# Optimization experiments

Measured on AMD Instinct MI355X. Metric: run time of the kernel, lower is better.

## Reference

```python
import jax, jax.numpy as jnp
import numpy as np

TOP_K = 2
EPS = 1e-9

def setup_inputs() -> dict:
    key = jax.random.key(0)
    ks = jax.random.split(key, 8)
    B, L, C, F = 64, 512, 3, 300          # batteries, cycles, channels, curve length
    d_model, d_llm, d_ff, E = 512, 4096, 2048, 8
    s = lambda k, sh: jax.random.normal(k, sh, jnp.float32) * 0.02
    return dict(
        cycle_curve_data=jax.random.normal(ks[0], (B, L, C, F), jnp.float32),
        cycle_numbers=jax.random.uniform(ks[1], (B, 1), jnp.float32),
        DKP_embeddings=jax.random.normal(ks[2], (B, d_llm), jnp.float32),
        gate_W1=s(ks[3], (d_llm + 1, d_ff)), gate_b1=jnp.zeros((d_ff,), jnp.float32),
        gate_W2=s(ks[4], (d_ff, E)), gate_b2=jnp.zeros((E,), jnp.float32),
        expert_W=s(ks[5], (E, C * F, d_model)), expert_b=jnp.zeros((E, d_model), jnp.float32),
        gen_W=s(ks[6], (C * F, d_model)), gen_b=jnp.zeros((d_model,), jnp.float32),
    )

def reference(cycle_curve_data, cycle_numbers, DKP_embeddings,
              gate_W1, gate_b1, gate_W2, gate_b2,
              expert_W, expert_b, gen_W, gen_b):
    B, L, C, F = cycle_curve_data.shape
    # router (PatternRouter_two): 2-layer MLP over [DKP embedding ; cycle number]
    g_in = jnp.concatenate([DKP_embeddings, cycle_numbers], axis=-1)   # [B, d_llm+1]
    h = jax.nn.gelu(g_in @ gate_W1 + gate_b1)
    logits = h @ gate_W2 + gate_b2                                     # [B, E]
    # top-k mask on raw logits (as in source), softmax, mask, renormalize
    _, idx = jax.lax.top_k(logits, TOP_K)
    mask = jnp.zeros(logits.shape, bool).at[jnp.arange(B)[:, None], idx].set(True)
    p = jax.nn.softmax(logits, axis=1)
    g = jnp.where(mask, p, 0.0)
    gates = g / (jnp.sum(g, axis=1, keepdims=True) + EPS)              # [B, E]
    # experts: flatten(start_dim=2) then Linear(3*F -> d_model); combine is linear
    # so fold gates into a per-battery weight: sum_e gates[b,e] * W_e
    x = cycle_curve_data.reshape(B, L, C * F)                          # [B, L, 3F]
    Wb = jnp.einsum('be,eid->bid', gates, expert_W)                    # [B, 3F, d]
    bb = gates @ expert_b                                              # [B, d]
    moe_out = jnp.einsum('bli,bid->bld', x, Wb) + bb[:, None, :]       # [B, L, d]
    general = x @ gen_W + gen_b                                        # [B, L, d]
    # source casts the combined MoE output to bf16 before adding
    return general + moe_out.astype(jnp.bfloat16)
```

## Files before the change

kernel.cpp:

```cpp
#include <hip/hip_runtime.h>
#include <hip/hip_bf16.h>
#include <stdint.h>

typedef __attribute__((ext_vector_type(8))) short short8;
typedef __attribute__((ext_vector_type(4))) short short4v;
typedef __attribute__((ext_vector_type(4))) float f32x4;

__device__ inline unsigned short f2bf(float f) {
    union { float f; uint32_t u; } v; v.f = f;
    uint32_t u = v.u;
    uint32_t r = (u + 0x7FFFu + ((u >> 16) & 1u)) >> 16;
    return (unsigned short)r;
}

__device__ inline short4v pk4(float4 a) {
    short4v r;
    r[0] = (short)f2bf(a.x); r[1] = (short)f2bf(a.y);
    r[2] = (short)f2bf(a.z); r[3] = (short)f2bf(a.w);
    return r;
}

__global__ __launch_bounds__(256) void router1(const float* __restrict__ DKP,
                                               const float* __restrict__ W1,
                                               float* __restrict__ part) {
    __shared__ float gin[16 * 64];
    const int t  = threadIdx.x;
    const int lin = blockIdx.x + 16 * blockIdx.y;
    const int bg  = (lin >> 3) & 3;
    const int grp = (lin & 7) | ((lin >> 5) << 3);
    const int jc  = grp & 3;
    const int ks  = grp >> 2;
    const int k0 = ks * 64;
    {
        const int b = t >> 4, q = t & 15;
        *(float4*)(gin + b * 64 + q * 4) =
            *(const float4*)(DKP + (size_t)(bg * 16 + b) * 4096 + k0 + q * 4);
    }
    __syncthreads();
    const int ja = jc * 512 + t, jb = ja + 256;
    float accA[16], accB[16];
    #pragma unroll
    for (int b = 0; b < 16; ++b) { accA[b] = 0.f; accB[b] = 0.f; }
    #pragma unroll 1
    for (int oct = 0; oct < 8; ++oct) {
        const int kk = oct * 8;
        float wa[8], wb[8];
        #pragma unroll
        for (int i = 0; i < 8; ++i) {
            const float* wr = W1 + (size_t)(k0 + kk + i) * 2048;
            wa[i] = wr[ja]; wb[i] = wr[jb];
        }
        #pragma unroll
        for (int b = 0; b < 16; ++b) {
            float4 g0 = *(const float4*)(gin + b * 64 + kk);
            float4 g1 = *(const float4*)(gin + b * 64 + kk + 4);
            accA[b] += g0.x*wa[0] + g0.y*wa[1] + g0.z*wa[2] + g0.w*wa[3]
                     + g1.x*wa[4] + g1.y*wa[5] + g1.z*wa[6] + g1.w*wa[7];
            accB[b] += g0.x*wb[0] + g0.y*wb[1] + g0.z*wb[2] + g0.w*wb[3]
                     + g1.x*wb[4] + g1.y*wb[5] + g1.z*wb[6] + g1.w*wb[7];
        }
    }
    #pragma unroll 1
    for (int b = 0; b < 16; ++b) {
        const size_t row = (size_t)(ks * 64 + bg * 16 + b) * 2048;
        part[row + ja] = accA[b];
        part[row + jb] = accB[b];
    }
}

__global__ __launch_bounds__(256) void router2(const float* __restrict__ part,
                                               const float* __restrict__ cyc,
                                               const float* __restrict__ W1,
                                               const float* __restrict__ b1,
                                               float* __restrict__ h) {
    const int idx = blockIdx.x * 256 + threadIdx.x;
    const int j = idx & 2047, b = idx >> 11;
    float s = 0.f;
    #pragma unroll 8
    for (int t = 0; t < 64; ++t)
        s += part[((size_t)t * 64 + b) * 2048 + j];
    s += cyc[b] * W1[(size_t)4096 * 2048 + j] + b1[j];
    const float u  = s + 0.044715f * s * s * s;
    const float th = tanhf(0.7978845608028654f * u);
    h[idx] = 0.5f * s * (1.0f + th);
}

__global__ __launch_bounds__(256) void router3(const float* __restrict__ h,
                                               const float* __restrict__ W2,
                                               const float* __restrict__ b2,
                                               float4* __restrict__ gates) {
    __shared__ float red[256 * 8];
    __shared__ float lg[8];
    const int b = blockIdx.x, t = threadIdx.x;
    float acc[8];
    #pragma unroll
    for (int e = 0; e < 8; ++e) acc[e] = 0.f;
    for (int k = t; k < 2048; k += 256) {
        const float hv = h[(size_t)b * 2048 + k];
        const float* w = W2 + (size_t)k * 8;
        #pragma unroll
        for (int e = 0; e < 8; ++e) acc[e] += hv * w[e];
    }
    #pragma unroll
    for (int e = 0; e < 8; ++e) red[t * 8 + e] = acc[e];
    __syncthreads();
    if (t < 8) {
        float s = 0.f;
        for (int r = 0; r < 256; ++r) s += red[r * 8 + t];
        lg[t] = s + b2[t];
    }
    __syncthreads();
    if (t == 0) {
        float l[8];
        #pragma unroll
        for (int e = 0; e < 8; ++e) l[e] = lg[e];
        int e0 = 0;
        #pragma unroll
        for (int e = 1; e < 8; ++e) if (l[e] > l[e0]) e0 = e;
        int e1 = (e0 == 0) ? 1 : 0;
        #pragma unroll
        for (int e = 0; e < 8; ++e) if (e != e0 && l[e] > l[e1]) e1 = e;
        const float m = l[e0];
        float p[8], Z = 0.f;
        #pragma unroll
        for (int e = 0; e < 8; ++e) { p[e] = expf(l[e] - m); Z += p[e]; }
        const float pe0 = p[e0] / Z, pe1 = p[e1] / Z;
        const float s2 = pe0 + pe1 + 1e-9f;
        gates[b] = make_float4(__int_as_float(e0), __int_as_float(e1), pe0 / s2, pe1 / s2);
    }
}

__global__ __launch_bounds__(256) void combine_w(const float* __restrict__ genW,
                                                 const float* __restrict__ expW,
                                                 const float4* __restrict__ gates,
                                                 unsigned short* __restrict__ wc) {
    __shared__ unsigned short T[64 * 72];
    const int b  = blockIdx.z;
    const int i0 = blockIdx.y * 64;
    const int d0 = blockIdx.x * 64;
    const float4 gt = gates[b];
    const int e0 = __float_as_int(gt.x), e1 = __float_as_int(gt.y);
    const float g0 = gt.z, g1 = gt.w;
    const float* W0 = expW + (size_t)e0 * 900 * 512;
    const float* W1e = expW + (size_t)e1 * 900 * 512;
    const int t = threadIdx.x;
    {
        const int il = t >> 2, c = t & 3;
        const int i = i0 + il;
        const bool valid = (i < 900);
        const size_t rowoff = (size_t)i * 512 + d0 + c * 16;
        #pragma unroll
        for (int s = 0; s < 4; ++s) {
            float4 g  = valid ? *(const float4*)(genW + rowoff + 4 * s) : make_float4(0,0,0,0);
            float4 w0 = valid ? *(const float4*)(W0   + rowoff + 4 * s) : make_float4(0,0,0,0);
            float4 w1 = valid ? *(const float4*)(W1e  + rowoff + 4 * s) : make_float4(0,0,0,0);
            const int dl = c * 16 + 4 * s;
            T[(dl + 0) * 72 + il] = f2bf(g.x + g0 * w0.x + g1 * w1.x);
            T[(dl + 1) * 72 + il] = f2bf(g.y + g0 * w0.y + g1 * w1.y);
            T[(dl + 2) * 72 + il] = f2bf(g.z + g0 * w0.z + g1 * w1.z);
            T[(dl + 3) * 72 + il] = f2bf(g.w + g0 * w0.w + g1 * w1.w);
        }
    }
    __syncthreads();
    {
        const int dl = t >> 2, seg = t & 3;
        const int ic = seg * 16;
        if (i0 + ic < 928) {
            short8 v0 = *(const short8*)&T[dl * 72 + ic];
            short8 v1 = *(const short8*)&T[dl * 72 + ic + 8];
            unsigned short* dst = wc + (size_t)b * 512 * 928 + (size_t)(d0 + dl) * 928 + i0 + ic;
            *(short8*)dst = v0;
            *((short8*)dst + 1) = v1;
        }
    }
}

__global__ __launch_bounds__(512, 4) void moe_gemm(const float* __restrict__ x,
                                                   const unsigned short* __restrict__ wc,
                                                   const float4* __restrict__ gates,
                                                   const float* __restrict__ eb,
                                                   const float* __restrict__ genb,
                                                   float* __restrict__ out) {
    __shared__ unsigned short As[2][64 * 40];
    __shared__ unsigned short Bs[2][512 * 32];
    const int b  = blockIdx.x;
    const int m0 = blockIdx.y * 64;
    const int t = threadIdx.x, lane = t & 63, wid = t >> 6;
    const float4 gt = gates[b];
    const int e0 = __float_as_int(gt.x), e1 = __float_as_int(gt.y);
    const float g0 = gt.z, g1 = gt.w;
    const float* xb = x + (size_t)b * 512 * 900;
    const unsigned short* wcb = wc + (size_t)b * 512 * 928;
    f32x4 acc[4][4];
    #pragma unroll
    for (int mi = 0; mi < 4; ++mi)
        #pragma unroll
        for (int ni = 0; ni < 4; ++ni)
            acc[mi][ni] = (f32x4){0.f, 0.f, 0.f, 0.f};

    const int arow  = t >> 3;
    const int akoff = (t & 7) * 4;
    const float* xrow = xb + (size_t)(m0 + arow) * 900 + akoff;
    const int bseg = (lane & 3) ^ ((lane >> 3) & 3);
    const int burow = lane >> 2;

    const int wn = wid * 64;
    const int lm = lane & 15, lq = lane >> 4;

    auto loadA = [&](int kt) -> float4 {
        if (kt < 28) return *(const float4*)(xrow + kt * 32);
        float4 z = make_float4(0.f, 0.f, 0.f, 0.f);
        if (akoff == 0) z = *(const float4*)(xrow + 896);
        return z;
    };
    auto stageB = [&](int buf, int kt) {
        const int k0 = kt * 32;
        #pragma unroll
        for (int r = 0; r < 4; ++r) {
            const int chunk = wid * 4 + r;
            const int n = chunk * 16 + burow;
            const unsigned short* gsrc = wcb + (size_t)n * 928 + k0 + bseg * 8;
            unsigned short* ldst = &Bs[buf][chunk * 512];
            __builtin_amdgcn_global_load_lds(
                (const __attribute__((address_space(1))) unsigned int*)gsrc,
                (__attribute__((address_space(3))) unsigned int*)ldst, 16, 0, 0);
        }
    };
    auto packA = [&](int buf, float4 f) {
        *(short4v*)&As[buf][arow * 40 + akoff] = pk4(f);
    };
    auto compute = [&](int buf) {
        short8 af[4], bfr[4];
        #pragma unroll
        for (int mi = 0; mi < 4; ++mi)
            af[mi] = *(const short8*)&As[buf][(mi * 16 + lm) * 40 + lq * 8];
        #pragma unroll
        for (int ni = 0; ni < 4; ++ni) {
            const int n = wn + ni * 16 + lm;
            const int slot = lq ^ ((lm >> 1) & 3);
            bfr[ni] = *(const short8*)&Bs[buf][n * 32 + slot * 8];
        }
        #pragma unroll
        for (int mi = 0; mi < 4; ++mi)
            #pragma unroll
            for (int ni = 0; ni < 4; ++ni)
                acc[mi][ni] = __builtin_amdgcn_mfma_f32_16x16x32_bf16(
                    af[mi], bfr[ni], acc[mi][ni], 0, 0, 0);
    };

    {
        float4 a0 = loadA(0);
        stageB(0, 0);
        packA(0, a0);
        __syncthreads();
    }
    #pragma unroll 1
    for (int kt2 = 0; kt2 < 14; ++kt2) {
        {
            float4 an = loadA(2 * kt2 + 1);
            stageB(1, 2 * kt2 + 1);
            compute(0);
            packA(1, an);
            __syncthreads();
        }
        {
            float4 an = loadA(2 * kt2 + 2);
            stageB(0, 2 * kt2 + 2);
            compute(1);
            packA(0, an);
            __syncthreads();
        }
    }
    compute(0);

    #pragma unroll
    for (int ni = 0; ni < 4; ++ni) {
        const int col = wn + ni * 16 + lm;
        const float bias = genb[col] + g0 * eb[e0 * 512 + col] + g1 * eb[e1 * 512 + col];
        #pragma unroll
        for (int mi = 0; mi < 4; ++mi) {
            const int row = m0 + mi * 16 + lq * 4;
            #pragma unroll
            for (int r = 0; r < 4; ++r)
                out[((size_t)b * 512 + row + r) * 512 + col] = acc[mi][ni][r] + bias;
        }
    }
}

extern "C" void kernel_launch(void* const* d_in, const int* in_sizes, int n_in,
                              void* d_out, int out_size, void* d_ws, size_t ws_size,
                              hipStream_t stream) {
    const float* x    = (const float*)d_in[0];
    const float* cyc  = (const float*)d_in[1];
    const float* dkp  = (const float*)d_in[2];
    const float* gW1  = (const float*)d_in[3];
    const float* gb1  = (const float*)d_in[4];
    const float* gW2  = (const float*)d_in[5];
    const float* gb2  = (const float*)d_in[6];
    const float* eW   = (const float*)d_in[7];
    const float* eb   = (const float*)d_in[8];
    const float* genW = (const float*)d_in[9];
    const float* genb = (const float*)d_in[10];
    float* out = (float*)d_out;

    char* ws = (char*)d_ws;
    unsigned short* wcomb = (unsigned short*)ws;
    float* part  = (float*)ws;
    float* h     = (float*)(ws + 60817408);
    float4* gts  = (float4*)(ws + 60817408 + 524288);

    router1<<<dim3(16, 64), 256, 0, stream>>>(dkp, gW1, part);
    router2<<<512, 256, 0, stream>>>(part, cyc, gW1, gb1, h);
    router3<<<64, 256, 0, stream>>>(h, gW2, gb2, gts);
    combine_w<<<dim3(8, 15, 64), 256, 0, stream>>>(genW, eW, gts, wcomb);
    moe_gemm<<<dim3(64, 8), 512, 0, stream>>>(x, wcomb, gts, eb, genb, out);
}
```

Measured before the change: 376.3 us.

## Fuse router stages, reuse expert weights across batches, and pipeline MoE GEMM waits

The router's first stage now uses deeper K slices (fewer partial sums), and the reduction/GELU stage is fused into the logits/top-k kernel, removing one launch and the h buffer. The weight-combine kernel loads all nine weight matrices for a tile once into shared memory and loops over all 64 batteries, instead of re-reading global weights per battery. The MoE GEMM main loop replaces __syncthreads with explicit s_waitcnt vmcnt(1) barriers plus sched_barriers, prefetching A two tiles ahead so global loads overlap compute. The risks are fewer router blocks for parallelism, higher shared memory use in combine_w, and hand-written waitcnt logic that could hide a race.

```diff
diff --git a/kernel.cpp b/kernel.cpp
--- a/kernel.cpp
+++ b/kernel.cpp
@@ -23,81 +23,70 @@
 __global__ __launch_bounds__(256) void router1(const float* __restrict__ DKP,
                                                const float* __restrict__ W1,
                                                float* __restrict__ part) {
-    __shared__ float gin[16 * 64];
-    const int t  = threadIdx.x;
+    __shared__ float gin[16 * 256];
+    const int t   = threadIdx.x;
     const int lin = blockIdx.x + 16 * blockIdx.y;
+    const int jc  = lin & 7;
     const int bg  = (lin >> 3) & 3;
-    const int grp = (lin & 7) | ((lin >> 5) << 3);
-    const int jc  = grp & 3;
-    const int ks  = grp >> 2;
-    const int k0 = ks * 64;
+    const int ks  = lin >> 5;
+    const int k0  = ks * 256;
     {
         const int b = t >> 4, q = t & 15;
-        *(float4*)(gin + b * 64 + q * 4) =
-            *(const float4*)(DKP + (size_t)(bg * 16 + b) * 4096 + k0 + q * 4);
+        #pragma unroll
+        for (int s = 0; s < 4; ++s)
+            *(float4*)(gin + b * 256 + q * 16 + s * 4) =
+                *(const float4*)(DKP + (size_t)(bg * 16 + b) * 4096 + k0 + q * 16 + s * 4);
     }
     __syncthreads();
-    const int ja = jc * 512 + t, jb = ja + 256;
-    float accA[16], accB[16];
-    #pragma unroll
-    for (int b = 0; b < 16; ++b) { accA[b] = 0.f; accB[b] = 0.f; }
-    #pragma unroll 1
-    for (int oct = 0; oct < 8; ++oct) {
+    const int ja = jc * 256 + t;
+    float accA[16];
+    #pragma unroll
+    for (int b = 0; b < 16; ++b) accA[b] = 0.f;
+    #pragma unroll 1
+    for (int oct = 0; oct < 32; ++oct) {
         const int kk = oct * 8;
-        float wa[8], wb[8];
-        #pragma unroll
-        for (int i = 0; i < 8; ++i) {
-            const float* wr = W1 + (size_t)(k0 + kk + i) * 2048;
-            wa[i] = wr[ja]; wb[i] = wr[jb];
-        }
+        float wa[8];
+        #pragma unroll
+        for (int i = 0; i < 8; ++i)
+            wa[i] = W1[(size_t)(k0 + kk + i) * 2048 + ja];
         #pragma unroll
         for (int b = 0; b < 16; ++b) {
-            float4 g0 = *(const float4*)(gin + b * 64 + kk);
-            float4 g1 = *(const float4*)(gin + b * 64 + kk + 4);
+            float4 g0 = *(const float4*)(gin + b * 256 + kk);
+            float4 g1 = *(const float4*)(gin + b * 256 + kk + 4);
             accA[b] += g0.x*wa[0] + g0.y*wa[1] + g0.z*wa[2] + g0.w*wa[3]
                      + g1.x*wa[4] + g1.y*wa[5] + g1.z*wa[6] + g1.w*wa[7];
-            accB[b] += g0.x*wb[0] + g0.y*wb[1] + g0.z*wb[2] + g0.w*wb[3]
-                     + g1.x*wb[4] + g1.y*wb[5] + g1.z*wb[6] + g1.w*wb[7];
-        }
-    }
-    #pragma unroll 1
-    for (int b = 0; b < 16; ++b) {
-        const size_t row = (size_t)(ks * 64 + bg * 16 + b) * 2048;
-        part[row + ja] = accA[b];
-        part[row + jb] = accB[b];
-    }
-}
-
-__global__ __launch_bounds__(256) void router2(const float* __restrict__ part,
-                                               const float* __restrict__ cyc,
-                                               const float* __restrict__ W1,
-                                               const float* __restrict__ b1,
-                                               float* __restrict__ h) {
-    const int idx = blockIdx.x * 256 + threadIdx.x;
-    const int j = idx & 2047, b = idx >> 11;
-    float s = 0.f;
-    #pragma unroll 8
-    for (int t = 0; t < 64; ++t)
-        s += part[((size_t)t * 64 + b) * 2048 + j];
-    s += cyc[b] * W1[(size_t)4096 * 2048 + j] + b1[j];
-    const float u  = s + 0.044715f * s * s * s;
-    const float th = tanhf(0.7978845608028654f * u);
-    h[idx] = 0.5f * s * (1.0f + th);
-}
-
-__global__ __launch_bounds__(256) void router3(const float* __restrict__ h,
-                                               const float* __restrict__ W2,
-                                               const float* __restrict__ b2,
-                                               float4* __restrict__ gates) {
+        }
+    }
+    #pragma unroll 1
+    for (int b = 0; b < 16; ++b)
+        part[((size_t)(ks * 64 + bg * 16 + b)) * 2048 + ja] = accA[b];
+}
+
+__global__ __launch_bounds__(256) void router23(const float* __restrict__ part,
+                                                const float* __restrict__ cyc,
+                                                const float* __restrict__ W1,
+                                                const float* __restrict__ b1,
+                                                const float* __restrict__ W2,
+                                                const float* __restrict__ b2,
+                                                float4* __restrict__ gates) {
     __shared__ float red[256 * 8];
     __shared__ float lg[8];
     const int b = blockIdx.x, t = threadIdx.x;
     float acc[8];
     #pragma unroll
     for (int e = 0; e < 8; ++e) acc[e] = 0.f;
-    for (int k = t; k < 2048; k += 256) {
-        const float hv = h[(size_t)b * 2048 + k];
-        const float* w = W2 + (size_t)k * 8;
+    #pragma unroll 1
+    for (int jj = 0; jj < 8; ++jj) {
+        const int j = jj * 256 + t;
+        float s = 0.f;
+        #pragma unroll
+        for (int tt = 0; tt < 16; ++tt)
+            s += part[((size_t)tt * 64 + b) * 2048 + j];
+        s += cyc[b] * W1[(size_t)4096 * 2048 + j] + b1[j];
+        const float u  = s + 0.044715f * s * s * s;
+        const float th = tanhf(0.7978845608028654f * u);
+        const float hv = 0.5f * s * (1.0f + th);
+        const float* w = W2 + (size_t)j * 8;
         #pragma unroll
         for (int e = 0; e < 8; ++e) acc[e] += hv * w[e];
     }
@@ -134,44 +123,46 @@
                                                  const float* __restrict__ expW,
                                                  const float4* __restrict__ gates,
                                                  unsigned short* __restrict__ wc) {
-    __shared__ unsigned short T[64 * 72];
-    const int b  = blockIdx.z;
-    const int i0 = blockIdx.y * 64;
-    const int d0 = blockIdx.x * 64;
-    const float4 gt = gates[b];
-    const int e0 = __float_as_int(gt.x), e1 = __float_as_int(gt.y);
-    const float g0 = gt.z, g1 = gt.w;
-    const float* W0 = expW + (size_t)e0 * 900 * 512;
-    const float* W1e = expW + (size_t)e1 * 900 * 512;
-    const int t = threadIdx.x;
+    __shared__ float T[9][32 * 36];
+    __shared__ float4 gsh[64];
+    const int t  = threadIdx.x;
+    const int d0 = blockIdx.x * 32;
+    const int i0 = blockIdx.y * 32;
+    if (t < 64) gsh[t] = gates[t];
     {
-        const int il = t >> 2, c = t & 3;
+        const int il = t >> 3, d4 = (t & 7) * 4;
         const int i = i0 + il;
         const bool valid = (i < 900);
-        const size_t rowoff = (size_t)i * 512 + d0 + c * 16;
-        #pragma unroll
-        for (int s = 0; s < 4; ++s) {
-            float4 g  = valid ? *(const float4*)(genW + rowoff + 4 * s) : make_float4(0,0,0,0);
-            float4 w0 = valid ? *(const float4*)(W0   + rowoff + 4 * s) : make_float4(0,0,0,0);
-            float4 w1 = valid ? *(const float4*)(W1e  + rowoff + 4 * s) : make_float4(0,0,0,0);
-            const int dl = c * 16 + 4 * s;
-            T[(dl + 0) * 72 + il] = f2bf(g.x + g0 * w0.x + g1 * w1.x);
-            T[(dl + 1) * 72 + il] = f2bf(g.y + g0 * w0.y + g1 * w1.y);
-            T[(dl + 2) * 72 + il] = f2bf(g.z + g0 * w0.z + g1 * w1.z);
-            T[(dl + 3) * 72 + il] = f2bf(g.w + g0 * w0.w + g1 * w1.w);
+        const size_t off = (size_t)i * 512 + d0 + d4;
+        #pragma unroll
+        for (int s = 0; s < 9; ++s) {
+            const float* src = (s == 0) ? genW : (expW + (size_t)(s - 1) * 900 * 512);
+            float4 v = valid ? *(const float4*)(src + off) : make_float4(0, 0, 0, 0);
+            float* Td = &T[s][0];
+            Td[(d4 + 0) * 36 + il] = v.x;
+            Td[(d4 + 1) * 36 + il] = v.y;
+            Td[(d4 + 2) * 36 + il] = v.z;
+            Td[(d4 + 3) * 36 + il] = v.w;
         }
     }
     __syncthreads();
-    {
-        const int dl = t >> 2, seg = t & 3;
-        const int ic = seg * 16;
-        if (i0 + ic < 928) {
-            short8 v0 = *(const short8*)&T[dl * 72 + ic];
-            short8 v1 = *(const short8*)&T[dl * 72 + ic + 8];
-            unsigned short* dst = wc + (size_t)b * 512 * 928 + (size_t)(d0 + dl) * 928 + i0 + ic;
-            *(short8*)dst = v0;
-            *((short8*)dst + 1) = v1;
-        }
+    const int dl = t >> 3, sg = t & 7;
+    const int fo = dl * 36 + sg * 4;
+    unsigned short* wrow = wc + (size_t)(d0 + dl) * 928 + i0 + sg * 4;
+    #pragma unroll 1
+    for (int b = 0; b < 64; ++b) {
+        const float4 gt = gsh[b];
+        const int e0 = __float_as_int(gt.x), e1 = __float_as_int(gt.y);
+        const float g0 = gt.z, g1 = gt.w;
+        float4 G = *(const float4*)&T[0][fo];
+        float4 X = *(const float4*)&T[1 + e0][fo];
+        float4 Y = *(const float4*)&T[1 + e1][fo];
+        short4v r;
+        r[0] = (short)f2bf(G.x + g0 * X.x + g1 * Y.x);
+        r[1] = (short)f2bf(G.y + g0 * X.y + g1 * Y.y);
+        r[2] = (short)f2bf(G.z + g0 * X.z + g1 * Y.z);
+        r[3] = (short)f2bf(G.w + g0 * X.w + g1 * Y.w);
+        *(short4v*)(wrow + (size_t)b * 512 * 928) = r;
     }
 }
 
@@ -248,30 +239,64 @@
                     af[mi], bfr[ni], acc[mi][ni], 0, 0, 0);
     };
 
+#define BAR_V1() do { \
+    asm volatile("s_waitcnt vmcnt(1) lgkmcnt(0)\n\ts_barrier" ::: "memory"); \
+    __builtin_amdgcn_sched_barrier(0); } while (0)
+#define BAR_V0() do { \
+    asm volatile("s_waitcnt vmcnt(0) lgkmcnt(0)\n\ts_barrier" ::: "memory"); \
+    __builtin_amdgcn_sched_barrier(0); } while (0)
+
+    stageB(0, 0);
+    __builtin_amdgcn_sched_barrier(0);
+    float4 a_cur  = loadA(0);
+    float4 a_next = loadA(1);
+    packA(0, a_cur);
+    BAR_V1();
+
+    #pragma unroll 1
+    for (int p = 0; p < 13; ++p) {
+        {
+            stageB(1, 2 * p + 1);
+            __builtin_amdgcn_sched_barrier(0);
+            float4 a2 = loadA(2 * p + 2);
+            __builtin_amdgcn_sched_barrier(0);
+            compute(0);
+            packA(1, a_next);
+            a_next = a2;
+            BAR_V1();
+        }
+        {
+            stageB(0, 2 * p + 2);
+            __builtin_amdgcn_sched_barrier(0);
+            float4 a2 = loadA(2 * p + 3);
+            __builtin_amdgcn_sched_barrier(0);
+            compute(1);
+            packA(0, a_next);
+            a_next = a2;
+            BAR_V1();
+        }
+    }
     {
-        float4 a0 = loadA(0);
-        stageB(0, 0);
-        packA(0, a0);
-        __syncthreads();
-    }
-    #pragma unroll 1
-    for (int kt2 = 0; kt2 < 14; ++kt2) {
-        {
-            float4 an = loadA(2 * kt2 + 1);
-            stageB(1, 2 * kt2 + 1);
-            compute(0);
-            packA(1, an);
-            __syncthreads();
-        }
-        {
-            float4 an = loadA(2 * kt2 + 2);
-            stageB(0, 2 * kt2 + 2);
-            compute(1);
-            packA(0, an);
-            __syncthreads();
-        }
+        stageB(1, 27);
+        __builtin_amdgcn_sched_barrier(0);
+        float4 a2 = loadA(28);
+        __builtin_amdgcn_sched_barrier(0);
+        compute(0);
+        packA(1, a_next);
+        a_next = a2;
+        BAR_V1();
+    }
+    {
+        stageB(0, 28);
+        __builtin_amdgcn_sched_barrier(0);
+        compute(1);
+        packA(0, a_next);
+        BAR_V0();
     }
     compute(0);
+
+#undef BAR_V1
+#undef BAR_V0
 
     #pragma unroll
     for (int ni = 0; ni < 4; ++ni) {
@@ -306,12 +331,10 @@
     char* ws = (char*)d_ws;
     unsigned short* wcomb = (unsigned short*)ws;
     float* part  = (float*)ws;
-    float* h     = (float*)(ws + 60817408);
-    float4* gts  = (float4*)(ws + 60817408 + 524288);
-
-    router1<<<dim3(16, 64), 256, 0, stream>>>(dkp, gW1, part);
-    router2<<<512, 256, 0, stream>>>(part, cyc, gW1, gb1, h);
-    router3<<<64, 256, 0, stream>>>(h, gW2, gb2, gts);
-    combine_w<<<dim3(8, 15, 64), 256, 0, stream>>>(genW, eW, gts, wcomb);
+    float4* gts  = (float4*)(ws + 60817408);
+
+    router1<<<dim3(16, 32), 256, 0, stream>>>(dkp, gW1, part);
+    router23<<<64, 256, 0, stream>>>(part, cyc, gW1, gb1, gW2, gb2, gts);
+    combine_w<<<dim3(16, 29), 256, 0, stream>>>(genW, eW, gts, wcomb);
     moe_gemm<<<dim3(64, 8), 512, 0, stream>>>(x, wcomb, gts, eb, genb, out);
 }
```

Result: faster. 363.5 us (-3.4%).
